# Optimization experiments

Hardware: AMD Instinct MI355X
Metric: run time of the kernel (lower is better)

The kernel has to match this reference:

```python
import jax, jax.numpy as jnp
import numpy as np

EPS = 0.01       # perturbation radius (constructor arg)
MEAN = 0.1307    # MNIST normalize constants from the 'else' branch
SIGMA = 0.3081


def _get_bound(v, eps):
    # torch get_bound detaches eps before taking |.| and summing
    r = jnp.sum(jnp.abs(jax.lax.stop_gradient(eps)), axis=-1)
    return v + r, v - r


def _relu_zono(v, eps):
    # v: [N], eps: [N, E]. Append one fresh (zero) error column, as the torch code does.
    n = v.shape[0]
    eps = jnp.concatenate([eps, jnp.zeros((n, 1), eps.dtype)], axis=-1)  # [N, E+1]
    u, l = _get_bound(v, eps)
    denom = u - l  # = 2*sum|eps| >= 0; guard against 0 for non-crossing rows
    # slopes are created as Parameters = u/(u-l) on the first pass (detached leaf)
    slope = jax.lax.stop_gradient(u / jnp.where(denom == 0, 1.0, denom))
    # at init slope == base = u/(u-l), so the slope <= base branch is taken
    term = (1.0 - slope) * u * 0.5
    crossing = (u > 0) & (l < 0)
    dead = u <= 0
    # torch uses slope.data * values.data for the linear part, + term (term carries grad)
    v_cross = jax.lax.stop_gradient(slope * v) + term
    v_new = jnp.where(dead, 0.0, jnp.where(crossing, v_cross, v))
    eps_cross = jnp.concatenate([slope[:, None] * eps[:, :-1], term[:, None]], axis=-1)
    eps_new = jnp.where(dead[:, None], 0.0, jnp.where(crossing[:, None], eps_cross, eps))
    return v_new, eps_new


def _forward(inputs, W1, b1, W2, b2, W3, b3):
    # initial zonotope build (faithful to source: values = u + l, radii = values - l = u)
    upper = jnp.minimum(inputs + EPS, 1.0)   # upper - relu(upper - 1)
    lower = jnp.maximum(inputs - EPS, 0.0)   # relu(lower)
    values = upper + lower
    eps = jnp.diag((values - lower).flatten())  # [D, D]
    # Normalize layer (the 'else' branch)
    values = (values - MEAN) / SIGMA
    eps = eps / SIGMA
    # Flatten
    v = values.flatten()
    # Linear -> ReLU -> Linear -> ReLU -> Linear
    v = W1 @ v + b1
    eps = W1 @ eps
    v, eps = _relu_zono(v, eps)
    v = W2 @ v + b2
    eps = W2 @ eps
    v, eps = _relu_zono(v, eps)
    v = W3 @ v + b3
    eps = W3 @ eps
    u, l = _get_bound(v, eps)
    return u, l


def setup_inputs() -> dict:
    key = jax.random.key(0)
    ks = jax.random.split(key, 7)
    D, H, O = 1024, 4096, 10
    inputs = jax.random.uniform(ks[0], (1, 1, 32, 32), jnp.float32)
    W1 = jax.random.normal(ks[1], (H, D), jnp.float32) / np.float32(np.sqrt(D))
    b1 = jax.random.normal(ks[2], (H,), jnp.float32) * 0.01
    W2 = jax.random.normal(ks[3], (H, H), jnp.float32) / np.float32(np.sqrt(H))
    b2 = jax.random.normal(ks[4], (H,), jnp.float32) * 0.01
    W3 = jax.random.normal(ks[5], (O, H), jnp.float32) / np.float32(np.sqrt(H))
    b3 = jax.random.normal(ks[6], (O,), jnp.float32) * 0.01
    return {"inputs": inputs, "W1": W1, "b1": b1, "W2": W2, "b2": b2, "W3": W3, "b3": b3}


def reference(inputs, W1, b1, W2, b2, W3, b3):
    return _forward(inputs, W1, b1, W2, b2, W3, b3)
```

## Files before the change

kernel.cpp:

```cpp
#include <hip/hip_runtime.h>
#include <math.h>

#define ZEPS  0.01f
#define ZMEAN 0.1307f
#define ZSIGMA 0.3081f

constexpr int D = 1024, H = 4096, O = 10;
constexpr size_t HD = (size_t)H * D;

using short8  = __attribute__((ext_vector_type(8))) short;
using ushort8 = __attribute__((ext_vector_type(8))) unsigned short;
using f32x4   = __attribute__((ext_vector_type(4))) float;
typedef unsigned short ushort_t;

__device__ inline unsigned short f2bf(float x) {
    unsigned int u = __float_as_uint(x);
    u += 0x7FFFu + ((u >> 16) & 1u);
    return (unsigned short)(u >> 16);
}
__device__ inline float bf2f(unsigned short h) {
    return __uint_as_float(((unsigned int)h) << 16);
}
__device__ inline unsigned int f2bf2_fast(float a, float b) {
    unsigned int ua = __float_as_uint(a) + 0x8000u;
    unsigned int ub = __float_as_uint(b) + 0x8000u;
    return (ua >> 16) | (ub & 0xFFFF0000u);
}

__device__ inline void gl_lds16(const void* g, void* l) {
    __builtin_amdgcn_global_load_lds(
        (const __attribute__((address_space(1))) unsigned int*)g,
        (__attribute__((address_space(3))) unsigned int*)l, 16, 0, 0);
}

__device__ inline float zval(float xv) {
    float up = fminf(xv + ZEPS, 1.f);
    float lo = fmaxf(xv - ZEPS, 0.f);
    return (up + lo - ZMEAN) / ZSIGMA;
}
__device__ inline float zdia(float xv) {
    return fminf(xv + ZEPS, 1.f) / ZSIGMA;
}

__device__ inline void relu_params(float v, float r, float& vout, float& aout, float& tout) {
    float u = v + r, l = v - r;
    float denom = u - l;
    float slope = u / (denom == 0.f ? 1.f : denom);
    float term = (1.f - slope) * u * 0.5f;
    bool dead = (u <= 0.f);
    bool crossing = (u > 0.f) && (l < 0.f);
    vout = dead ? 0.f : (crossing ? (slope * v + term) : v);
    aout = dead ? 0.f : (crossing ? slope : 1.f);
    tout = (!dead && crossing) ? term : 0.f;
}

__global__ __launch_bounds__(256) void k_layer1(const float* __restrict__ W1, const float* __restrict__ b1,
                                                const float* __restrict__ x,
                                                float* __restrict__ v1p, float* __restrict__ a1,
                                                float* __restrict__ t1) {
    int wid = threadIdx.x >> 6, lane = threadIdx.x & 63;
    int i = blockIdx.x * 4 + wid;
    const float* row = W1 + (size_t)i * D;
    float sv = 0.f, sr = 0.f;
#pragma unroll
    for (int it = 0; it < 4; ++it) {
        int j = it * 256 + lane * 4;
        float4 w = *(const float4*)&row[j];
        float4 xx = *(const float4*)&x[j];
        sv += w.x * zval(xx.x) + w.y * zval(xx.y) + w.z * zval(xx.z) + w.w * zval(xx.w);
        sr += fabsf(w.x) * zdia(xx.x) + fabsf(w.y) * zdia(xx.y) +
              fabsf(w.z) * zdia(xx.z) + fabsf(w.w) * zdia(xx.w);
    }
#pragma unroll
    for (int m = 1; m <= 32; m <<= 1) {
        sv += __shfl_xor(sv, m, 64);
        sr += __shfl_xor(sr, m, 64);
    }
    if (lane == 0) {
        float vo, ao, to;
        relu_params(sv + b1[i], sr, vo, ao, to);
        v1p[i] = vo; a1[i] = ao; t1[i] = to;
    }
}

__global__ __launch_bounds__(256) void k_scaleT(const float* __restrict__ W1, const float* __restrict__ a1,
                                                const float* __restrict__ x,
                                                ushort_t* __restrict__ W1sT) {
    __shared__ float tile[32][33];
    int j0 = blockIdx.x * 32, k0 = blockIdx.y * 32;
    int r = threadIdx.x >> 3;
    int c = (threadIdx.x & 7) * 4;
    float4 w = *(const float4*)&W1[(size_t)(k0 + r) * D + j0 + c];
    float4 xx = *(const float4*)&x[j0 + c];
    float a = a1[k0 + r];
    tile[r][c + 0] = a * w.x * zdia(xx.x);
    tile[r][c + 1] = a * w.y * zdia(xx.y);
    tile[r][c + 2] = a * w.z * zdia(xx.z);
    tile[r][c + 3] = a * w.w * zdia(xx.w);
    __syncthreads();
    ushort4 o;
    o.x = f2bf(tile[c + 0][r]);
    o.y = f2bf(tile[c + 1][r]);
    o.z = f2bf(tile[c + 2][r]);
    o.w = f2bf(tile[c + 3][r]);
    *(ushort4*)&W1sT[(size_t)(j0 + r) * H + k0 + c] = o;
}

#define GBK 64
__global__ __launch_bounds__(256) void k_gemm_mfma(const float* __restrict__ A,
                                                   const ushort_t* __restrict__ B,
                                                   const float* __restrict__ v1p,
                                                   const float* __restrict__ t1,
                                                   ushort_t* __restrict__ C,
                                                   float* __restrict__ vpart,
                                                   float* __restrict__ tpart) {
    const int N = D, K = H;
    __shared__ __align__(16) ushort_t As[2][128 * GBK];
    __shared__ __align__(16) ushort_t Bs[2][128 * GBK];
    __shared__ float vt[2048], tt[2048];
    int b = blockIdx.x;
    int u = b & 7, v = b >> 3;
    int z = u >> 2;
    int y = (u & 3) * 8 + (v >> 3);
    int xb = v & 7;
    int tid = threadIdx.x;
    int wave = tid >> 6, lane = tid & 63;
    int bm = y * 128, bn = xb * 128;
    int kbeg = z * (K / 2);
    ushort_t* Cz = C + (size_t)z * HD;
    int wm = (wave >> 1) * 64, wn = (wave & 1) * 64;

    int srow = lane >> 3, sc = lane & 7, scp = sc ^ srow;
    int r15 = lane & 15, quad = lane >> 4, key = r15 & 7;
    int rowg = tid >> 3, ch = tid & 7;
    int aswz = ch ^ (rowg & 7);

    const int S = (K / 2) / GBK;

    float4 pa[4][2];
    float sv[4] = {0.f, 0.f, 0.f, 0.f}, st[4] = {0.f, 0.f, 0.f, 0.f};

    auto issueA = [&](int s) {
#pragma unroll
        for (int g = 0; g < 4; ++g) {
            const float* ap = &A[(size_t)(bm + g * 32 + rowg) * K + kbeg + s * GBK + ch * 8];
            pa[g][0] = *(const float4*)ap;
            pa[g][1] = *(const float4*)(ap + 4);
        }
    };
    auto issueB = [&](int s, int buf) {
#pragma unroll
        for (int g = 0; g < 4; ++g) {
            int row = wave * 32 + g * 8;
            gl_lds16(&B[(size_t)(bn + row + srow) * K + kbeg + s * GBK + scp * 8], &Bs[buf][row * GBK]);
        }
    };
    auto cvtwrite = [&](int s, int buf) {
        if ((s & 7) == xb) {
            const float* vp = &vt[s * 64 + ch * 8];
            const float* tp = &tt[s * 64 + ch * 8];
            float4 v0 = *(const float4*)vp, v1 = *(const float4*)(vp + 4);
            float4 t0 = *(const float4*)tp, t1v = *(const float4*)(tp + 4);
#pragma unroll
            for (int g = 0; g < 4; ++g) {
                sv[g] += pa[g][0].x * v0.x + pa[g][0].y * v0.y + pa[g][0].z * v0.z + pa[g][0].w * v0.w
                       + pa[g][1].x * v1.x + pa[g][1].y * v1.y + pa[g][1].z * v1.z + pa[g][1].w * v1.w;
                st[g] += pa[g][0].x * t0.x + pa[g][0].y * t0.y + pa[g][0].z * t0.z + pa[g][0].w * t0.w
                       + pa[g][1].x * t1v.x + pa[g][1].y * t1v.y + pa[g][1].z * t1v.z + pa[g][1].w * t1v.w;
            }
        }
#pragma unroll
        for (int g = 0; g < 4; ++g) {
            uint4 hh;
            hh.x = f2bf2_fast(pa[g][0].x, pa[g][0].y);
            hh.y = f2bf2_fast(pa[g][0].z, pa[g][0].w);
            hh.z = f2bf2_fast(pa[g][1].x, pa[g][1].y);
            hh.w = f2bf2_fast(pa[g][1].z, pa[g][1].w);
            *(uint4*)&As[buf][(g * 32 + rowg) * GBK + aswz * 8] = hh;
        }
    };

    f32x4 acc[4][4];
#pragma unroll
    for (int p = 0; p < 4; ++p)
#pragma unroll
        for (int q = 0; q < 4; ++q) acc[p][q] = (f32x4){0.f, 0.f, 0.f, 0.f};

    issueA(0);
    issueB(0, 0);
    for (int idx = tid; idx < 512; idx += 256) {
        *(float4*)&vt[idx * 4] = *(const float4*)&v1p[kbeg + idx * 4];
        *(float4*)&tt[idx * 4] = *(const float4*)&t1[kbeg + idx * 4];
    }
    __syncthreads();
    cvtwrite(0, 0);
    __syncthreads();

    for (int s = 0; s < S; ++s) {
        int buf = s & 1, nbuf = buf ^ 1;
        if (s + 1 < S) {
            issueA(s + 1);
            issueB(s + 1, nbuf);
        }
#pragma unroll
        for (int kk = 0; kk < 2; ++kk) {
            short8 af[4], bf[4];
#pragma unroll
            for (int mt = 0; mt < 4; ++mt)
                af[mt] = *(const short8*)&As[buf][(wm + mt * 16 + r15) * GBK + (((kk * 4 + quad) ^ key)) * 8];
#pragma unroll
            for (int nt = 0; nt < 4; ++nt)
                bf[nt] = *(const short8*)&Bs[buf][(wn + nt * 16 + r15) * GBK + (((kk * 4 + quad) ^ key)) * 8];
#pragma unroll
            for (int mt = 0; mt < 4; ++mt)
#pragma unroll
                for (int nt = 0; nt < 4; ++nt)
                    acc[mt][nt] = __builtin_amdgcn_mfma_f32_16x16x32_bf16(af[mt], bf[nt], acc[mt][nt], 0, 0, 0);
        }
        if (s + 1 < S) cvtwrite(s + 1, nbuf);
        __syncthreads();
    }

#pragma unroll
    for (int mt = 0; mt < 4; ++mt) {
        int gr = bm + wm + mt * 16 + quad * 4;
#pragma unroll
        for (int nt = 0; nt < 4; ++nt) {
            int gc = bn + wn + nt * 16 + r15;
            Cz[(size_t)(gr + 0) * N + gc] = f2bf(acc[mt][nt][0]);
            Cz[(size_t)(gr + 1) * N + gc] = f2bf(acc[mt][nt][1]);
            Cz[(size_t)(gr + 2) * N + gc] = f2bf(acc[mt][nt][2]);
            Cz[(size_t)(gr + 3) * N + gc] = f2bf(acc[mt][nt][3]);
        }
    }

#pragma unroll
    for (int g = 0; g < 4; ++g) {
        float a = sv[g], bb = st[g];
        a += __shfl_xor(a, 1, 64); a += __shfl_xor(a, 2, 64); a += __shfl_xor(a, 4, 64);
        bb += __shfl_xor(bb, 1, 64); bb += __shfl_xor(bb, 2, 64); bb += __shfl_xor(bb, 4, 64);
        if (ch == 0) {
            int i = bm + g * 32 + rowg;
            vpart[(size_t)(z * 8 + xb) * H + i] = a;
            tpart[(size_t)(z * 8 + xb) * H + i] = bb;
        }
    }
}

__global__ __launch_bounds__(256) void k_mid(const ushort_t* __restrict__ e1, const ushort_t* __restrict__ e2,
                                             const float* __restrict__ vpart, const float* __restrict__ tpart,
                                             const float* __restrict__ b2, const float* __restrict__ W3,
                                             float* __restrict__ v2p, float* __restrict__ a2,
                                             float* __restrict__ t2, float* __restrict__ t2col,
                                             float* __restrict__ pbuf) {
    __shared__ float sa2[16];
    __shared__ float sw3[16][O];
    int blk = blockIdx.x, tid = threadIdx.x;
    int wave = tid >> 6, lane = tid & 63;

#pragma unroll
    for (int r = 0; r < 4; ++r) {
        int ii = wave * 4 + r;
        int i = blk * 16 + ii;
        size_t off = (size_t)i * D + lane * 16;
        ushort8 a0 = *(const ushort8*)&e1[off];
        ushort8 a1v = *(const ushort8*)&e1[off + 8];
        ushort8 b0 = *(const ushort8*)&e2[off];
        ushort8 b1v = *(const ushort8*)&e2[off + 8];
        float s = 0.f;
#pragma unroll
        for (int q = 0; q < 8; ++q)
            s += fabsf(bf2f(a0[q]) + bf2f(b0[q])) + fabsf(bf2f(a1v[q]) + bf2f(b1v[q]));
        float ve = (lane < 16) ? vpart[(size_t)lane * H + i] : 0.f;
        float te = (lane < 16) ? tpart[(size_t)lane * H + i] : 0.f;
#pragma unroll
        for (int m = 1; m <= 32; m <<= 1) {
            s += __shfl_xor(s, m, 64);
            ve += __shfl_xor(ve, m, 64);
            te += __shfl_xor(te, m, 64);
        }
        if (lane == 0) {
            float vo, ao, to;
            relu_params(ve + b2[i], s + fabsf(te), vo, ao, to);
            v2p[i] = vo; a2[i] = ao; t2[i] = to; t2col[i] = te; sa2[ii] = ao;
        }
    }
    __syncthreads();
    if (tid < 16 * O) {
        int ii = tid / O, o = tid % O;
        sw3[ii][o] = W3[(size_t)o * H + blk * 16 + ii] * sa2[ii];
    }
    __syncthreads();

    int j = tid * 4;
    float acc[4][O];
#pragma unroll
    for (int c = 0; c < 4; ++c)
#pragma unroll
        for (int o = 0; o < O; ++o) acc[c][o] = 0.f;
#pragma unroll
    for (int ii = 0; ii < 16; ++ii) {
        size_t off = (size_t)(blk * 16 + ii) * D + j;
        ushort4 za = *(const ushort4*)&e1[off];
        ushort4 zb = *(const ushort4*)&e2[off];
        float e0 = bf2f(za.x) + bf2f(zb.x);
        float ee1 = bf2f(za.y) + bf2f(zb.y);
        float ee2 = bf2f(za.z) + bf2f(zb.z);
        float ee3 = bf2f(za.w) + bf2f(zb.w);
        const float* w = sw3[ii];
#pragma unroll
        for (int o = 0; o < O; ++o) {
            float wo = w[o];
            acc[0][o] += wo * e0; acc[1][o] += wo * ee1;
            acc[2][o] += wo * ee2; acc[3][o] += wo * ee3;
        }
    }
#pragma unroll
    for (int o = 0; o < O; ++o) {
        float4 stv = make_float4(acc[0][o], acc[1][o], acc[2][o], acc[3][o]);
        *(float4*)&pbuf[((size_t)o * 256 + blk) * D + j] = stv;
    }
}

__global__ __launch_bounds__(1024) void k_final(const float* __restrict__ W3, const float* __restrict__ b3,
                                                const float* __restrict__ v2p, const float* __restrict__ a2,
                                                const float* __restrict__ t2col, const float* __restrict__ t2,
                                                const float* __restrict__ pbuf, float* __restrict__ out) {
    int o = blockIdx.x, tid = threadIdx.x;
    float t = 0.f;
    const float* pb = pbuf + (size_t)o * 256 * D;
    for (int s = 0; s < 256; ++s) t += pb[(size_t)s * D + tid];
    float s3 = fabsf(t);

    const float* row = W3 + (size_t)o * H;
    float sv = 0.f, s1 = 0.f, s2 = 0.f;
#pragma unroll
    for (int it = 0; it < 4; ++it) {
        int i = it * 1024 + tid;
        float w = row[i];
        sv += w * v2p[i];
        s1 += w * a2[i] * t2col[i];
        s2 += w * t2[i];
    }
    __shared__ float red[4][1024];
    red[0][tid] = sv; red[1][tid] = s1; red[2][tid] = s2; red[3][tid] = s3;
    __syncthreads();
    for (int off2 = 512; off2; off2 >>= 1) {
        if (tid < off2) {
            red[0][tid] += red[0][tid + off2];
            red[1][tid] += red[1][tid + off2];
            red[2][tid] += red[2][tid + off2];
            red[3][tid] += red[3][tid + off2];
        }
        __syncthreads();
    }
    if (tid == 0) {
        float v3 = red[0][0] + b3[o];
        float rr = red[3][0] + fabsf(red[1][0]) + fabsf(red[2][0]);
        out[o] = v3 + rr;
        out[O + o] = v3 - rr;
    }
}

extern "C" void kernel_launch(void* const* d_in, const int* in_sizes, int n_in,
                              void* d_out, int out_size, void* d_ws, size_t ws_size,
                              hipStream_t stream) {
    const float* x  = (const float*)d_in[0];
    const float* W1 = (const float*)d_in[1];
    const float* b1 = (const float*)d_in[2];
    const float* W2 = (const float*)d_in[3];
    const float* b2 = (const float*)d_in[4];
    const float* W3 = (const float*)d_in[5];
    const float* b3 = (const float*)d_in[6];
    float* out = (float*)d_out;

    float* p = (float*)d_ws;
    float* v1p   = p; p += H;
    float* a1    = p; p += H;
    float* t1    = p; p += H;
    float* t2col = p; p += H;
    float* v2p   = p; p += H;
    float* a2    = p; p += H;
    float* t2    = p; p += H;
    float* vpart = p; p += 16 * H;
    float* tpart = p; p += 16 * H;
    float* pbuf  = p; p += (size_t)O * 256 * D;
    ushort_t* eps2 = (ushort_t*)p;
    ushort_t* W1sT = eps2 + 2 * HD;
    ushort_t* eps2b = eps2 + HD;

    k_layer1<<<H / 4, 256, 0, stream>>>(W1, b1, x, v1p, a1, t1);
    k_scaleT<<<dim3(D / 32, H / 32), 256, 0, stream>>>(W1, a1, x, W1sT);
    k_gemm_mfma<<<512, 256, 0, stream>>>(W2, W1sT, v1p, t1, eps2, vpart, tpart);
    k_mid<<<256, 256, 0, stream>>>(eps2, eps2b, vpart, tpart, b2, W3, v2p, a2, t2, t2col, pbuf);
    k_final<<<O, 1024, 0, stream>>>(W3, b3, v2p, a2, t2col, t2, pbuf, out);
}
```

Measured before the change: 210.0 us.

## Pre-convert W2 to bf16 in separate pass, enlarge GEMM tiles, split final reduction

Adds a k_conv kernel that computes the W2·v1 and W2·t1 matvecs and writes W2 as bf16, so the GEMM no longer converts fp32 A on the fly or computes partial matvecs. The GEMM now uses 128x256 tiles with single-buffered LDS loads through global_load_lds for both operands, 256 blocks, and launch_bounds occupancy 2. The final reduction is split across 8x10 blocks with atomics and a last-block finalize. This costs an extra full read of W2 plus a bf16 write and re-read, and drops the previous double-buffered prefetch overlap.

New measurement: 207.0 us. No clear change (-1.4%).

```diff
diff --git a/kernel.cpp b/kernel.cpp
--- a/kernel.cpp
+++ b/kernel.cpp
@@ -20,11 +20,6 @@
 }
 __device__ inline float bf2f(unsigned short h) {
     return __uint_as_float(((unsigned int)h) << 16);
-}
-__device__ inline unsigned int f2bf2_fast(float a, float b) {
-    unsigned int ua = __float_as_uint(a) + 0x8000u;
-    unsigned int ub = __float_as_uint(b) + 0x8000u;
-    return (ua >> 16) | (ub & 0xFFFF0000u);
 }
 
 __device__ inline void gl_lds16(const void* g, void* l) {
@@ -57,7 +52,8 @@
 __global__ __launch_bounds__(256) void k_layer1(const float* __restrict__ W1, const float* __restrict__ b1,
                                                 const float* __restrict__ x,
                                                 float* __restrict__ v1p, float* __restrict__ a1,
-                                                float* __restrict__ t1) {
+                                                float* __restrict__ t1, float* __restrict__ sbuf) {
+    if (blockIdx.x == 0 && threadIdx.x < 96) sbuf[threadIdx.x] = 0.f;
     int wid = threadIdx.x >> 6, lane = threadIdx.x & 63;
     int i = blockIdx.x * 4 + wid;
     const float* row = W1 + (size_t)i * D;
@@ -106,118 +102,91 @@
     *(ushort4*)&W1sT[(size_t)(j0 + r) * H + k0 + c] = o;
 }
 
+__global__ __launch_bounds__(256) void k_conv(const float* __restrict__ W2, const float* __restrict__ b2,
+                                              const float* __restrict__ v1p, const float* __restrict__ t1,
+                                              float* __restrict__ v2, float* __restrict__ t2col,
+                                              ushort_t* __restrict__ W2b) {
+    __shared__ float vt[4096], tt[4096];
+    int tid = threadIdx.x, wave = tid >> 6, lane = tid & 63;
+    for (int idx = tid; idx < 1024; idx += 256) {
+        *(float4*)&vt[idx * 4] = *(const float4*)&v1p[idx * 4];
+        *(float4*)&tt[idx * 4] = *(const float4*)&t1[idx * 4];
+    }
+    __syncthreads();
+    int i = blockIdx.x * 4 + wave;
+    const float* row = W2 + (size_t)i * H;
+    ushort_t* orow = W2b + (size_t)i * H;
+    float sv = 0.f, st = 0.f;
+#pragma unroll 4
+    for (int it = 0; it < 16; ++it) {
+        int j = it * 256 + lane * 4;
+        float4 w = *(const float4*)&row[j];
+        float4 vv = *(const float4*)&vt[j];
+        float4 tv = *(const float4*)&tt[j];
+        sv += w.x * vv.x + w.y * vv.y + w.z * vv.z + w.w * vv.w;
+        st += w.x * tv.x + w.y * tv.y + w.z * tv.z + w.w * tv.w;
+        ushort4 o;
+        o.x = f2bf(w.x); o.y = f2bf(w.y); o.z = f2bf(w.z); o.w = f2bf(w.w);
+        *(ushort4*)&orow[j] = o;
+    }
+#pragma unroll
+    for (int m = 1; m <= 32; m <<= 1) { sv += __shfl_xor(sv, m, 64); st += __shfl_xor(st, m, 64); }
+    if (lane == 0) { v2[i] = sv + b2[i]; t2col[i] = st; }
+}
+
 #define GBK 64
-__global__ __launch_bounds__(256) void k_gemm_mfma(const float* __restrict__ A,
-                                                   const ushort_t* __restrict__ B,
-                                                   const float* __restrict__ v1p,
-                                                   const float* __restrict__ t1,
-                                                   ushort_t* __restrict__ C,
-                                                   float* __restrict__ vpart,
-                                                   float* __restrict__ tpart) {
-    const int N = D, K = H;
-    __shared__ __align__(16) ushort_t As[2][128 * GBK];
-    __shared__ __align__(16) ushort_t Bs[2][128 * GBK];
-    __shared__ float vt[2048], tt[2048];
+__global__ __launch_bounds__(256, 2) void k_gemm_mfma(const ushort_t* __restrict__ A,
+                                                      const ushort_t* __restrict__ B,
+                                                      ushort_t* __restrict__ C) {
+    const int K = H;
+    __shared__ __align__(16) ushort_t As[128 * GBK];
+    __shared__ __align__(16) ushort_t Bs[256 * GBK];
     int b = blockIdx.x;
     int u = b & 7, v = b >> 3;
-    int z = u >> 2;
-    int y = (u & 3) * 8 + (v >> 3);
-    int xb = v & 7;
+    int t = u * 8 + (v >> 2);
+    int z = t >> 5, y = t & 31, xb = v & 3;
     int tid = threadIdx.x;
     int wave = tid >> 6, lane = tid & 63;
-    int bm = y * 128, bn = xb * 128;
-    int kbeg = z * (K / 2);
+    int bm = y * 128, bn = xb * 256, kbeg = z * 2048;
     ushort_t* Cz = C + (size_t)z * HD;
-    int wm = (wave >> 1) * 64, wn = (wave & 1) * 64;
-
+    int wm = (wave >> 1) * 64, wn = (wave & 1) * 128;
     int srow = lane >> 3, sc = lane & 7, scp = sc ^ srow;
     int r15 = lane & 15, quad = lane >> 4, key = r15 & 7;
-    int rowg = tid >> 3, ch = tid & 7;
-    int aswz = ch ^ (rowg & 7);
-
-    const int S = (K / 2) / GBK;
-
-    float4 pa[4][2];
-    float sv[4] = {0.f, 0.f, 0.f, 0.f}, st[4] = {0.f, 0.f, 0.f, 0.f};
-
-    auto issueA = [&](int s) {
-#pragma unroll
-        for (int g = 0; g < 4; ++g) {
-            const float* ap = &A[(size_t)(bm + g * 32 + rowg) * K + kbeg + s * GBK + ch * 8];
-            pa[g][0] = *(const float4*)ap;
-            pa[g][1] = *(const float4*)(ap + 4);
-        }
-    };
-    auto issueB = [&](int s, int buf) {
+
+    f32x4 acc[4][8];
+#pragma unroll
+    for (int p = 0; p < 4; ++p)
+#pragma unroll
+        for (int q = 0; q < 8; ++q) acc[p][q] = (f32x4){0.f, 0.f, 0.f, 0.f};
+
+    for (int s = 0; s < 32; ++s) {
+        int k0 = kbeg + s * GBK;
 #pragma unroll
         for (int g = 0; g < 4; ++g) {
             int row = wave * 32 + g * 8;
-            gl_lds16(&B[(size_t)(bn + row + srow) * K + kbeg + s * GBK + scp * 8], &Bs[buf][row * GBK]);
-        }
-    };
-    auto cvtwrite = [&](int s, int buf) {
-        if ((s & 7) == xb) {
-            const float* vp = &vt[s * 64 + ch * 8];
-            const float* tp = &tt[s * 64 + ch * 8];
-            float4 v0 = *(const float4*)vp, v1 = *(const float4*)(vp + 4);
-            float4 t0 = *(const float4*)tp, t1v = *(const float4*)(tp + 4);
-#pragma unroll
-            for (int g = 0; g < 4; ++g) {
-                sv[g] += pa[g][0].x * v0.x + pa[g][0].y * v0.y + pa[g][0].z * v0.z + pa[g][0].w * v0.w
-                       + pa[g][1].x * v1.x + pa[g][1].y * v1.y + pa[g][1].z * v1.z + pa[g][1].w * v1.w;
-                st[g] += pa[g][0].x * t0.x + pa[g][0].y * t0.y + pa[g][0].z * t0.z + pa[g][0].w * t0.w
-                       + pa[g][1].x * t1v.x + pa[g][1].y * t1v.y + pa[g][1].z * t1v.z + pa[g][1].w * t1v.w;
-            }
-        }
-#pragma unroll
-        for (int g = 0; g < 4; ++g) {
-            uint4 hh;
-            hh.x = f2bf2_fast(pa[g][0].x, pa[g][0].y);
-            hh.y = f2bf2_fast(pa[g][0].z, pa[g][0].w);
-            hh.z = f2bf2_fast(pa[g][1].x, pa[g][1].y);
-            hh.w = f2bf2_fast(pa[g][1].z, pa[g][1].w);
-            *(uint4*)&As[buf][(g * 32 + rowg) * GBK + aswz * 8] = hh;
-        }
-    };
-
-    f32x4 acc[4][4];
-#pragma unroll
-    for (int p = 0; p < 4; ++p)
-#pragma unroll
-        for (int q = 0; q < 4; ++q) acc[p][q] = (f32x4){0.f, 0.f, 0.f, 0.f};
-
-    issueA(0);
-    issueB(0, 0);
-    for (int idx = tid; idx < 512; idx += 256) {
-        *(float4*)&vt[idx * 4] = *(const float4*)&v1p[kbeg + idx * 4];
-        *(float4*)&tt[idx * 4] = *(const float4*)&t1[kbeg + idx * 4];
-    }
-    __syncthreads();
-    cvtwrite(0, 0);
-    __syncthreads();
-
-    for (int s = 0; s < S; ++s) {
-        int buf = s & 1, nbuf = buf ^ 1;
-        if (s + 1 < S) {
-            issueA(s + 1);
-            issueB(s + 1, nbuf);
-        }
+            gl_lds16(&A[(size_t)(bm + row + srow) * K + k0 + scp * 8], &As[row * GBK]);
+        }
+#pragma unroll
+        for (int g = 0; g < 8; ++g) {
+            int row = wave * 64 + g * 8;
+            gl_lds16(&B[(size_t)(bn + row + srow) * K + k0 + scp * 8], &Bs[row * GBK]);
+        }
+        __syncthreads();
 #pragma unroll
         for (int kk = 0; kk < 2; ++kk) {
-            short8 af[4], bf[4];
+            short8 af[4], bf[8];
 #pragma unroll
             for (int mt = 0; mt < 4; ++mt)
-                af[mt] = *(const short8*)&As[buf][(wm + mt * 16 + r15) * GBK + (((kk * 4 + quad) ^ key)) * 8];
-#pragma unroll
-            for (int nt = 0; nt < 4; ++nt)
-                bf[nt] = *(const short8*)&Bs[buf][(wn + nt * 16 + r15) * GBK + (((kk * 4 + quad) ^ key)) * 8];
+                af[mt] = *(const short8*)&As[(wm + mt * 16 + r15) * GBK + ((kk * 4 + quad) ^ key) * 8];
+#pragma unroll
+            for (int nt = 0; nt < 8; ++nt)
+                bf[nt] = *(const short8*)&Bs[(wn + nt * 16 + r15) * GBK + ((kk * 4 + quad) ^ key) * 8];
 #pragma unroll
             for (int mt = 0; mt < 4; ++mt)
 #pragma unroll
-                for (int nt = 0; nt < 4; ++nt)
+                for (int nt = 0; nt < 8; ++nt)
                     acc[mt][nt] = __builtin_amdgcn_mfma_f32_16x16x32_bf16(af[mt], bf[nt], acc[mt][nt], 0, 0, 0);
         }
-        if (s + 1 < S) cvtwrite(s + 1, nbuf);
         __syncthreads();
     }
 
@@ -225,43 +194,31 @@
     for (int mt = 0; mt < 4; ++mt) {
         int gr = bm + wm + mt * 16 + quad * 4;
 #pragma unroll
-        for (int nt = 0; nt < 4; ++nt) {
+        for (int nt = 0; nt < 8; ++nt) {
             int gc = bn + wn + nt * 16 + r15;
-            Cz[(size_t)(gr + 0) * N + gc] = f2bf(acc[mt][nt][0]);
-            Cz[(size_t)(gr + 1) * N + gc] = f2bf(acc[mt][nt][1]);
-            Cz[(size_t)(gr + 2) * N + gc] = f2bf(acc[mt][nt][2]);
-            Cz[(size_t)(gr + 3) * N + gc] = f2bf(acc[mt][nt][3]);
-        }
-    }
-
-#pragma unroll
-    for (int g = 0; g < 4; ++g) {
-        float a = sv[g], bb = st[g];
-        a += __shfl_xor(a, 1, 64); a += __shfl_xor(a, 2, 64); a += __shfl_xor(a, 4, 64);
-        bb += __shfl_xor(bb, 1, 64); bb += __shfl_xor(bb, 2, 64); bb += __shfl_xor(bb, 4, 64);
-        if (ch == 0) {
-            int i = bm + g * 32 + rowg;
-            vpart[(size_t)(z * 8 + xb) * H + i] = a;
-            tpart[(size_t)(z * 8 + xb) * H + i] = bb;
+            Cz[(size_t)(gr + 0) * D + gc] = f2bf(acc[mt][nt][0]);
+            Cz[(size_t)(gr + 1) * D + gc] = f2bf(acc[mt][nt][1]);
+            Cz[(size_t)(gr + 2) * D + gc] = f2bf(acc[mt][nt][2]);
+            Cz[(size_t)(gr + 3) * D + gc] = f2bf(acc[mt][nt][3]);
         }
     }
 }
 
 __global__ __launch_bounds__(256) void k_mid(const ushort_t* __restrict__ e1, const ushort_t* __restrict__ e2,
-                                             const float* __restrict__ vpart, const float* __restrict__ tpart,
-                                             const float* __restrict__ b2, const float* __restrict__ W3,
+                                             const float* __restrict__ v2, const float* __restrict__ t2col,
+                                             const float* __restrict__ W3,
                                              float* __restrict__ v2p, float* __restrict__ a2,
-                                             float* __restrict__ t2, float* __restrict__ t2col,
-                                             float* __restrict__ pbuf) {
+                                             float* __restrict__ t2, float* __restrict__ pbuf) {
     __shared__ float sa2[16];
     __shared__ float sw3[16][O];
     int blk = blockIdx.x, tid = threadIdx.x;
     int wave = tid >> 6, lane = tid & 63;
+    int base = blk * 16;
 
 #pragma unroll
     for (int r = 0; r < 4; ++r) {
         int ii = wave * 4 + r;
-        int i = blk * 16 + ii;
+        int i = base + ii;
         size_t off = (size_t)i * D + lane * 16;
         ushort8 a0 = *(const ushort8*)&e1[off];
         ushort8 a1v = *(const ushort8*)&e1[off + 8];
@@ -271,24 +228,18 @@
 #pragma unroll
         for (int q = 0; q < 8; ++q)
             s += fabsf(bf2f(a0[q]) + bf2f(b0[q])) + fabsf(bf2f(a1v[q]) + bf2f(b1v[q]));
-        float ve = (lane < 16) ? vpart[(size_t)lane * H + i] : 0.f;
-        float te = (lane < 16) ? tpart[(size_t)lane * H + i] : 0.f;
-#pragma unroll
-        for (int m = 1; m <= 32; m <<= 1) {
-            s += __shfl_xor(s, m, 64);
-            ve += __shfl_xor(ve, m, 64);
-            te += __shfl_xor(te, m, 64);
-        }
+#pragma unroll
+        for (int m = 1; m <= 32; m <<= 1) s += __shfl_xor(s, m, 64);
         if (lane == 0) {
             float vo, ao, to;
-            relu_params(ve + b2[i], s + fabsf(te), vo, ao, to);
-            v2p[i] = vo; a2[i] = ao; t2[i] = to; t2col[i] = te; sa2[ii] = ao;
+            relu_params(v2[i], s + fabsf(t2col[i]), vo, ao, to);
+            v2p[i] = vo; a2[i] = ao; t2[i] = to; sa2[ii] = ao;
         }
     }
     __syncthreads();
     if (tid < 16 * O) {
         int ii = tid / O, o = tid % O;
-        sw3[ii][o] = W3[(size_t)o * H + blk * 16 + ii] * sa2[ii];
+        sw3[ii][o] = W3[(size_t)o * H + base + ii] * sa2[ii];
     }
     __syncthreads();
 
@@ -300,7 +251,7 @@
         for (int o = 0; o < O; ++o) acc[c][o] = 0.f;
 #pragma unroll
     for (int ii = 0; ii < 16; ++ii) {
-        size_t off = (size_t)(blk * 16 + ii) * D + j;
+        size_t off = (size_t)(base + ii) * D + j;
         ushort4 za = *(const ushort4*)&e1[off];
         ushort4 zb = *(const ushort4*)&e2[off];
         float e0 = bf2f(za.x) + bf2f(zb.x);
@@ -322,43 +273,64 @@
     }
 }
 
-__global__ __launch_bounds__(1024) void k_final(const float* __restrict__ W3, const float* __restrict__ b3,
+__global__ __launch_bounds__(128) void k_final2(const float* __restrict__ W3, const float* __restrict__ b3,
                                                 const float* __restrict__ v2p, const float* __restrict__ a2,
                                                 const float* __restrict__ t2col, const float* __restrict__ t2,
-                                                const float* __restrict__ pbuf, float* __restrict__ out) {
-    int o = blockIdx.x, tid = threadIdx.x;
-    float t = 0.f;
+                                                const float* __restrict__ pbuf, float* __restrict__ sbuf,
+                                                float* __restrict__ out) {
+    int g = blockIdx.x, o = blockIdx.y, tid = threadIdx.x;
+    int j = g * 128 + tid;
+    float tsum = 0.f;
     const float* pb = pbuf + (size_t)o * 256 * D;
-    for (int s = 0; s < 256; ++s) t += pb[(size_t)s * D + tid];
-    float s3 = fabsf(t);
+    for (int s = 0; s < 256; ++s) tsum += pb[(size_t)s * D + j];
+    float s3 = fabsf(tsum);
 
     const float* row = W3 + (size_t)o * H;
     float sv = 0.f, s1 = 0.f, s2 = 0.f;
 #pragma unroll
     for (int it = 0; it < 4; ++it) {
-        int i = it * 1024 + tid;
+        int i = g * 512 + it * 128 + tid;
         float w = row[i];
         sv += w * v2p[i];
         s1 += w * a2[i] * t2col[i];
         s2 += w * t2[i];
     }
-    __shared__ float red[4][1024];
-    red[0][tid] = sv; red[1][tid] = s1; red[2][tid] = s2; red[3][tid] = s3;
-    __syncthreads();
-    for (int off2 = 512; off2; off2 >>= 1) {
-        if (tid < off2) {
-            red[0][tid] += red[0][tid + off2];
-            red[1][tid] += red[1][tid + off2];
-            red[2][tid] += red[2][tid + off2];
-            red[3][tid] += red[3][tid + off2];
+    __shared__ float red[4][128];
+    red[0][tid] = s3; red[1][tid] = sv; red[2][tid] = s1; red[3][tid] = s2;
+    __syncthreads();
+    for (int off = 64; off; off >>= 1) {
+        if (tid < off) {
+            red[0][tid] += red[0][tid + off];
+            red[1][tid] += red[1][tid + off];
+            red[2][tid] += red[2][tid + off];
+            red[3][tid] += red[3][tid + off];
         }
         __syncthreads();
     }
+    __shared__ int isLast;
     if (tid == 0) {
-        float v3 = red[0][0] + b3[o];
-        float rr = red[3][0] + fabsf(red[1][0]) + fabsf(red[2][0]);
-        out[o] = v3 + rr;
-        out[O + o] = v3 - rr;
+        atomicAdd(&sbuf[o], red[0][0]);
+        atomicAdd(&sbuf[16 + o], red[1][0]);
+        atomicAdd(&sbuf[32 + o], red[2][0]);
+        atomicAdd(&sbuf[48 + o], red[3][0]);
+        __threadfence();
+        int old = atomicAdd((int*)&sbuf[64], 1);
+        isLast = (old == 8 * O - 1);
+    }
+    __syncthreads();
+    if (isLast) {
+        __threadfence();
+        if (tid < O) {
+            int o2 = tid;
+            float r3v = atomicAdd(&sbuf[o2], 0.f);
+            float dvv = atomicAdd(&sbuf[16 + o2], 0.f);
+            float d1v = atomicAdd(&sbuf[32 + o2], 0.f);
+            float d2v = atomicAdd(&sbuf[48 + o2], 0.f);
+            float v3 = dvv + b3[o2];
+            float rr = r3v + fabsf(d1v) + fabsf(d2v);
+            out[o2] = v3 + rr;
+            out[O + o2] = v3 - rr;
+        }
     }
 }
 
@@ -378,20 +350,23 @@
     float* v1p   = p; p += H;
     float* a1    = p; p += H;
     float* t1    = p; p += H;
+    float* v2    = p; p += H;
     float* t2col = p; p += H;
     float* v2p   = p; p += H;
     float* a2    = p; p += H;
     float* t2    = p; p += H;
-    float* vpart = p; p += 16 * H;
-    float* tpart = p; p += 16 * H;
+    float* sbuf  = p; p += 96;
+    p += 32;
     float* pbuf  = p; p += (size_t)O * 256 * D;
     ushort_t* eps2 = (ushort_t*)p;
     ushort_t* W1sT = eps2 + 2 * HD;
+    ushort_t* W2b  = W1sT + HD;
     ushort_t* eps2b = eps2 + HD;
 
-    k_layer1<<<H / 4, 256, 0, stream>>>(W1, b1, x, v1p, a1, t1);
+    k_layer1<<<H / 4, 256, 0, stream>>>(W1, b1, x, v1p, a1, t1, sbuf);
     k_scaleT<<<dim3(D / 32, H / 32), 256, 0, stream>>>(W1, a1, x, W1sT);
-    k_gemm_mfma<<<512, 256, 0, stream>>>(W2, W1sT, v1p, t1, eps2, vpart, tpart);
-    k_mid<<<256, 256, 0, stream>>>(eps2, eps2b, vpart, tpart, b2, W3, v2p, a2, t2, t2col, pbuf);
-    k_final<<<O, 1024, 0, stream>>>(W3, b3, v2p, a2, t2col, t2, pbuf, out);
-}
+    k_conv<<<H / 4, 256, 0, stream>>>(W2, b2, v1p, t1, v2, t2col, W2b);
+    k_gemm_mfma<<<256, 256, 0, stream>>>(W2b, W1sT, eps2);
+    k_mid<<<256, 256, 0, stream>>>(eps2, eps2b, v2, t2col, W3, v2p, a2, t2, pbuf);
+    k_final2<<<dim3(8, O), 128, 0, stream>>>(W3, b3, v2p, a2, t2col, t2, pbuf, sbuf, out);
+}
```
